# Kernel optimization log

Hardware: AMD Instinct MI355X
Metric: run time of the kernel (lower is better)

## Reference

```python
import jax, jax.numpy as jnp
import numpy as np

GROUP = 64

def dequant(W_q, scale, zero):
    # W_q: [out, in] int, scale/zero: [out, in//GROUP]
    out, din = W_q.shape
    g = din // GROUP
    Wq = W_q.reshape(out, g, GROUP).astype(scale.dtype)
    W = (Wq - zero[:, :, None]) * scale[:, :, None]
    return W.reshape(out, din)

def setup_inputs() -> dict:
    key = jax.random.key(0)
    ks = jax.random.split(key, 10)
    T, H, F = 512, 4096, 14336
    return {
        "hidden_states": jax.random.normal(ks[0], (T, H), jnp.float32),
        "W1_q": jax.random.randint(ks[1], (F, H), 0, 16, jnp.int32),
        "w1_scale": jax.random.uniform(ks[2], (F, H // GROUP), jnp.float32, 1e-3, 0.02),
        "w1_zero": jax.random.uniform(ks[3], (F, H // GROUP), jnp.float32, 6.0, 9.0),
        "W3_q": jax.random.randint(ks[4], (F, H), 0, 16, jnp.int32),
        "w3_scale": jax.random.uniform(ks[5], (F, H // GROUP), jnp.float32, 1e-3, 0.02),
        "w3_zero": jax.random.uniform(ks[6], (F, H // GROUP), jnp.float32, 6.0, 9.0),
        "W2_q": jax.random.randint(ks[7], (H, F), 0, 16, jnp.int32),
        "w2_scale": jax.random.uniform(ks[8], (H, F // GROUP), jnp.float32, 1e-3, 0.02),
        "w2_zero": jax.random.uniform(ks[9], (H, F // GROUP), jnp.float32, 6.0, 9.0),
    }

def reference(hidden_states, W1_q, w1_scale, w1_zero, W3_q, w3_scale, w3_zero, W2_q, w2_scale, w2_zero):
    W1 = dequant(W1_q, w1_scale, w1_zero)  # [F, H]
    W3 = dequant(W3_q, w3_scale, w3_zero)  # [F, H]
    W2 = dequant(W2_q, w2_scale, w2_zero)  # [H, F]
    g = jax.nn.silu(hidden_states @ W1.T) * (hidden_states @ W3.T)  # [T, F]
    return g @ W2.T  # [T, H]
```

## Files before the change

### kernel.cpp

```cpp
#include <hip/hip_runtime.h>
#include <hip/hip_bf16.h>

#define T_DIM 512
#define H_DIM 4096
#define F_DIM 14336
#define KSEG  8

typedef __attribute__((ext_vector_type(8))) short bf16x8;
typedef __attribute__((ext_vector_type(4))) float f32x4;

__device__ __forceinline__ unsigned short f2bf(float f) {
    union { __hip_bfloat16 h; unsigned short u; } cv;
    cv.h = __float2bfloat16(f);
    return cv.u;
}

__global__ __launch_bounds__(256) void zero_out(float4* __restrict__ out) {
    out[blockIdx.x * 256 + threadIdx.x] = make_float4(0.f, 0.f, 0.f, 0.f);
}

__global__ __launch_bounds__(256) void cvt_x(const float* __restrict__ X,
                                             unsigned short* __restrict__ Xb) {
    int i = (blockIdx.x * 256 + threadIdx.x) * 4;
    float4 v = *(const float4*)&X[i];
    ushort4 o;
    o.x = f2bf(v.x); o.y = f2bf(v.y); o.z = f2bf(v.z); o.w = f2bf(v.w);
    *(ushort4*)&Xb[i] = o;
}

__global__ __launch_bounds__(256, 2)
void gate_up_kernel(const unsigned short* __restrict__ Xb,
                    const int* __restrict__ W1q, const float* __restrict__ sc1,
                    const float* __restrict__ zp1,
                    const int* __restrict__ W3q, const float* __restrict__ sc3,
                    const float* __restrict__ zp3,
                    unsigned short* __restrict__ G)
{
    constexpr int LK = 72;
    __shared__ __align__(16) char smem[(128 + 64 + 64) * LK * 2];
    unsigned short* sX  = (unsigned short*)smem;
    unsigned short* sW1 = (unsigned short*)(smem + 128 * LK * 2);
    unsigned short* sW3 = (unsigned short*)(smem + 192 * LK * 2);
    float* sEx = (float*)smem;

    const int t = threadIdx.x, wave = t >> 6, lane = t & 63;
    const int r = lane & 15, q = lane >> 4;
    const int mh  = (wave & 1) * 64;
    const int mat = wave >> 1;

    const int b = blockIdx.x;
    const int xcd = b & 7, lb = b >> 3;
    const int m0 = (lb & 3) * 128;
    const int n0 = (xcd * 28 + (lb >> 2)) * 64;
    const int SG = H_DIM / 64;

    const int xrow = t >> 3, xch = (t & 7) * 8;
    const int wrow = t >> 4, wc = (t & 15) * 4;

    int4 pW1[4], pW3[4];
    #pragma unroll
    for (int i = 0; i < 4; ++i) {
        size_t off = (size_t)(n0 + wrow + 16 * i) * H_DIM + wc;
        pW1[i] = *(const int4*)&W1q[off];
        pW3[i] = *(const int4*)&W3q[off];
    }

    f32x4 acc[4][4];
    #pragma unroll
    for (int a = 0; a < 4; ++a)
        #pragma unroll
        for (int c = 0; c < 4; ++c) acc[a][c] = (f32x4){0.f, 0.f, 0.f, 0.f};

    for (int k0 = 0; k0 < H_DIM; k0 += 64) {
        const int gidx = k0 >> 6;

        #pragma unroll
        for (int i = 0; i < 4; ++i) {
            int4 xv = *(const int4*)&Xb[(size_t)(m0 + xrow + 32 * i) * H_DIM + k0 + xch];
            *(int4*)&sX[(xrow + 32 * i) * LK + xch] = xv;
        }
        #pragma unroll
        for (int i = 0; i < 4; ++i) {
            int row = wrow + 16 * i;
            int sidx = (n0 + row) * SG + gidx;
            float s = sc1[sidx], nzs = -zp1[sidx] * s;
            int4 qv = pW1[i];
            ushort4 o;
            o.x = f2bf(fmaf((float)qv.x, s, nzs)); o.y = f2bf(fmaf((float)qv.y, s, nzs));
            o.z = f2bf(fmaf((float)qv.z, s, nzs)); o.w = f2bf(fmaf((float)qv.w, s, nzs));
            *(ushort4*)&sW1[row * LK + wc] = o;
            s = sc3[sidx]; nzs = -zp3[sidx] * s;
            qv = pW3[i];
            o.x = f2bf(fmaf((float)qv.x, s, nzs)); o.y = f2bf(fmaf((float)qv.y, s, nzs));
            o.z = f2bf(fmaf((float)qv.z, s, nzs)); o.w = f2bf(fmaf((float)qv.w, s, nzs));
            *(ushort4*)&sW3[row * LK + wc] = o;
        }
        int kn = k0 + 64;
        if (kn < H_DIM) {
            #pragma unroll
            for (int i = 0; i < 4; ++i) {
                size_t off = (size_t)(n0 + wrow + 16 * i) * H_DIM + kn + wc;
                pW1[i] = *(const int4*)&W1q[off];
                pW3[i] = *(const int4*)&W3q[off];
            }
        }
        __syncthreads();

        const unsigned short* sB = mat ? sW3 : sW1;
        #pragma unroll
        for (int kh = 0; kh < 2; ++kh) {
            const int kb = kh * 32 + q * 8;
            bf16x8 av[4], bv[4];
            #pragma unroll
            for (int im = 0; im < 4; ++im)
                av[im] = *(const bf16x8*)&sX[(mh + im * 16 + r) * LK + kb];
            #pragma unroll
            for (int j = 0; j < 4; ++j)
                bv[j] = *(const bf16x8*)&sB[(j * 16 + r) * LK + kb];
            #pragma unroll
            for (int im = 0; im < 4; ++im)
                #pragma unroll
                for (int j = 0; j < 4; ++j)
                    acc[im][j] = __builtin_amdgcn_mfma_f32_16x16x32_bf16(av[im], bv[j], acc[im][j], 0, 0, 0);
        }
        __syncthreads();
    }

    if (mat == 1) {
        #pragma unroll
        for (int im = 0; im < 4; ++im)
            #pragma unroll
            for (int j = 0; j < 4; ++j)
                #pragma unroll
                for (int reg = 0; reg < 4; ++reg)
                    sEx[(mh + im * 16 + q * 4 + reg) * 65 + j * 16 + r] = acc[im][j][reg];
    }
    __syncthreads();
    if (mat == 0) {
        #pragma unroll
        for (int im = 0; im < 4; ++im)
            #pragma unroll
            for (int j = 0; j < 4; ++j)
                #pragma unroll
                for (int reg = 0; reg < 4; ++reg) {
                    int ml = mh + im * 16 + q * 4 + reg;
                    int nl = j * 16 + r;
                    float g1 = acc[im][j][reg];
                    float g3 = sEx[ml * 65 + nl];
                    float val = g1 / (1.f + __expf(-g1)) * g3;
                    G[(size_t)(m0 + ml) * F_DIM + n0 + nl] = f2bf(val);
                }
    }
}

__global__ __launch_bounds__(256, 2)
void down_kernel(const unsigned short* __restrict__ G,
                 const int* __restrict__ W2q, const float* __restrict__ sc2,
                 const float* __restrict__ zp2,
                 float* __restrict__ Out)
{
    constexpr int LK = 72;
    __shared__ __align__(16) char smem[(128 + 128) * LK * 2];
    unsigned short* sA = (unsigned short*)smem;
    unsigned short* sW = (unsigned short*)(smem + 128 * LK * 2);

    const int t = threadIdx.x, wave = t >> 6, lane = t & 63;
    const int r = lane & 15, q = lane >> 4;
    const int wm = (wave & 1) * 64, wn = (wave >> 1) * 64;

    const int b = blockIdx.x;
    const int xcd = b & 7, lb = b >> 3;
    const int m0 = (lb & 3) * 128;
    const int pair = xcd * 32 + (lb >> 2);
    const int n0 = (pair >> 3) * 128;
    const int kbeg = (pair & 7) * (F_DIM / KSEG);
    const int kend = kbeg + (F_DIM / KSEG);
    const int SG = F_DIM / 64;

    const int arow = t >> 3, ach = (t & 7) * 8;
    const int wrow = t >> 4, wc = (t & 15) * 4;

    int4 pW[8];
    #pragma unroll
    for (int i = 0; i < 8; ++i)
        pW[i] = *(const int4*)&W2q[(size_t)(n0 + wrow + 16 * i) * F_DIM + kbeg + wc];

    f32x4 acc[4][4];
    #pragma unroll
    for (int a = 0; a < 4; ++a)
        #pragma unroll
        for (int c = 0; c < 4; ++c) acc[a][c] = (f32x4){0.f, 0.f, 0.f, 0.f};

    for (int k0 = kbeg; k0 < kend; k0 += 64) {
        const int gidx = k0 >> 6;

        #pragma unroll
        for (int i = 0; i < 4; ++i) {
            int4 gv = *(const int4*)&G[(size_t)(m0 + arow + 32 * i) * F_DIM + k0 + ach];
            *(int4*)&sA[(arow + 32 * i) * LK + ach] = gv;
        }
        #pragma unroll
        for (int i = 0; i < 8; ++i) {
            int row = wrow + 16 * i;
            int sidx = (n0 + row) * SG + gidx;
            float s = sc2[sidx], nzs = -zp2[sidx] * s;
            int4 qv = pW[i];
            ushort4 o;
            o.x = f2bf(fmaf((float)qv.x, s, nzs)); o.y = f2bf(fmaf((float)qv.y, s, nzs));
            o.z = f2bf(fmaf((float)qv.z, s, nzs)); o.w = f2bf(fmaf((float)qv.w, s, nzs));
            *(ushort4*)&sW[row * LK + wc] = o;
        }
        int kn = k0 + 64;
        if (kn < kend) {
            #pragma unroll
            for (int i = 0; i < 8; ++i)
                pW[i] = *(const int4*)&W2q[(size_t)(n0 + wrow + 16 * i) * F_DIM + kn + wc];
        }
        __syncthreads();

        #pragma unroll
        for (int kh = 0; kh < 2; ++kh) {
            const int kb = kh * 32 + q * 8;
            bf16x8 av[4], bv[4];
            #pragma unroll
            for (int im = 0; im < 4; ++im)
                av[im] = *(const bf16x8*)&sA[(wm + im * 16 + r) * LK + kb];
            #pragma unroll
            for (int j = 0; j < 4; ++j)
                bv[j] = *(const bf16x8*)&sW[(wn + j * 16 + r) * LK + kb];
            #pragma unroll
            for (int im = 0; im < 4; ++im)
                #pragma unroll
                for (int j = 0; j < 4; ++j)
                    acc[im][j] = __builtin_amdgcn_mfma_f32_16x16x32_bf16(av[im], bv[j], acc[im][j], 0, 0, 0);
        }
        __syncthreads();
    }

    #pragma unroll
    for (int im = 0; im < 4; ++im)
        #pragma unroll
        for (int j = 0; j < 4; ++j)
            #pragma unroll
            for (int reg = 0; reg < 4; ++reg) {
                int m = m0 + wm + im * 16 + q * 4 + reg;
                int h = n0 + wn + j * 16 + r;
                atomicAdd(&Out[(size_t)m * H_DIM + h], acc[im][j][reg]);
            }
}

extern "C" void kernel_launch(void* const* d_in, const int* in_sizes, int n_in,
                              void* d_out, int out_size, void* d_ws, size_t ws_size,
                              hipStream_t stream) {
    const float* X   = (const float*)d_in[0];
    const int*   W1q = (const int*)d_in[1];
    const float* s1  = (const float*)d_in[2];
    const float* z1  = (const float*)d_in[3];
    const int*   W3q = (const int*)d_in[4];
    const float* s3  = (const float*)d_in[5];
    const float* z3  = (const float*)d_in[6];
    const int*   W2q = (const int*)d_in[7];
    const float* s2  = (const float*)d_in[8];
    const float* z2  = (const float*)d_in[9];
    float* Out = (float*)d_out;

    unsigned short* Xb = (unsigned short*)d_ws;
    unsigned short* G  = (unsigned short*)((char*)d_ws + (4 << 20));

    zero_out<<<2048, 256, 0, stream>>>((float4*)Out);
    cvt_x<<<2048, 256, 0, stream>>>(X, Xb);
    gate_up_kernel<<<896, 256, 0, stream>>>(Xb, W1q, s1, z1, W3q, s3, z3, G);
    down_kernel<<<1024, 256, 0, stream>>>(G, W2q, s2, z2, Out);
}
```

Measured before the change: 878.6 us.

## Double-buffer LDS tiles in gate/up and down kernels to drop one barrier

Both GEMM kernels now keep two shared-memory tile buffers. Each iteration computes MFMAs on the current buffer while loading and dequantizing the next tile into the other, so each K step needs one barrier instead of two. This should let dequant and global-load latency overlap with matrix math. It doubles LDS use per block (about 72KB for gate/up), which could limit occupancy under launch_bounds(256,2).

Measured after the change: 873.3 us. About the same (-0.6%).

```diff
diff --git a/kernel.cpp b/kernel.cpp
--- a/kernel.cpp
+++ b/kernel.cpp
@@ -13,6 +13,16 @@
     union { __hip_bfloat16 h; unsigned short u; } cv;
     cv.h = __float2bfloat16(f);
     return cv.u;
+}
+
+__device__ __forceinline__ void dq16(int4 qv, float s, float z, unsigned short* dst) {
+    float nzs = -z * s;
+    ushort4 o;
+    o.x = f2bf(fmaf((float)qv.x, s, nzs));
+    o.y = f2bf(fmaf((float)qv.y, s, nzs));
+    o.z = f2bf(fmaf((float)qv.z, s, nzs));
+    o.w = f2bf(fmaf((float)qv.w, s, nzs));
+    *(ushort4*)dst = o;
 }
 
 __global__ __launch_bounds__(256) void zero_out(float4* __restrict__ out) {
@@ -37,10 +47,8 @@
                     unsigned short* __restrict__ G)
 {
     constexpr int LK = 72;
-    __shared__ __align__(16) char smem[(128 + 64 + 64) * LK * 2];
-    unsigned short* sX  = (unsigned short*)smem;
-    unsigned short* sW1 = (unsigned short*)(smem + 128 * LK * 2);
-    unsigned short* sW3 = (unsigned short*)(smem + 192 * LK * 2);
+    constexpr int BUFB = (128 + 64 + 64) * LK * 2;
+    __shared__ __align__(16) char smem[2 * BUFB];
     float* sEx = (float*)smem;
 
     const int t = threadIdx.x, wave = t >> 6, lane = t & 63;
@@ -65,48 +73,45 @@
         pW3[i] = *(const int4*)&W3q[off];
     }
 
-    f32x4 acc[4][4];
-    #pragma unroll
-    for (int a = 0; a < 4; ++a)
-        #pragma unroll
-        for (int c = 0; c < 4; ++c) acc[a][c] = (f32x4){0.f, 0.f, 0.f, 0.f};
-
-    for (int k0 = 0; k0 < H_DIM; k0 += 64) {
-        const int gidx = k0 >> 6;
-
+    {
+        unsigned short* sX  = (unsigned short*)smem;
+        unsigned short* sW1 = (unsigned short*)(smem + 128 * LK * 2);
+        unsigned short* sW3 = (unsigned short*)(smem + 192 * LK * 2);
         #pragma unroll
         for (int i = 0; i < 4; ++i) {
-            int4 xv = *(const int4*)&Xb[(size_t)(m0 + xrow + 32 * i) * H_DIM + k0 + xch];
+            int4 xv = *(const int4*)&Xb[(size_t)(m0 + xrow + 32 * i) * H_DIM + xch];
             *(int4*)&sX[(xrow + 32 * i) * LK + xch] = xv;
         }
         #pragma unroll
         for (int i = 0; i < 4; ++i) {
             int row = wrow + 16 * i;
-            int sidx = (n0 + row) * SG + gidx;
-            float s = sc1[sidx], nzs = -zp1[sidx] * s;
-            int4 qv = pW1[i];
-            ushort4 o;
-            o.x = f2bf(fmaf((float)qv.x, s, nzs)); o.y = f2bf(fmaf((float)qv.y, s, nzs));
-            o.z = f2bf(fmaf((float)qv.z, s, nzs)); o.w = f2bf(fmaf((float)qv.w, s, nzs));
-            *(ushort4*)&sW1[row * LK + wc] = o;
-            s = sc3[sidx]; nzs = -zp3[sidx] * s;
-            qv = pW3[i];
-            o.x = f2bf(fmaf((float)qv.x, s, nzs)); o.y = f2bf(fmaf((float)qv.y, s, nzs));
-            o.z = f2bf(fmaf((float)qv.z, s, nzs)); o.w = f2bf(fmaf((float)qv.w, s, nzs));
-            *(ushort4*)&sW3[row * LK + wc] = o;
-        }
-        int kn = k0 + 64;
-        if (kn < H_DIM) {
-            #pragma unroll
-            for (int i = 0; i < 4; ++i) {
-                size_t off = (size_t)(n0 + wrow + 16 * i) * H_DIM + kn + wc;
-                pW1[i] = *(const int4*)&W1q[off];
-                pW3[i] = *(const int4*)&W3q[off];
-            }
-        }
-        __syncthreads();
-
-        const unsigned short* sB = mat ? sW3 : sW1;
+            int sidx = (n0 + row) * SG;
+            dq16(pW1[i], sc1[sidx], zp1[sidx], &sW1[row * LK + wc]);
+            dq16(pW3[i], sc3[sidx], zp3[sidx], &sW3[row * LK + wc]);
+        }
+        #pragma unroll
+        for (int i = 0; i < 4; ++i) {
+            size_t off = (size_t)(n0 + wrow + 16 * i) * H_DIM + 64 + wc;
+            pW1[i] = *(const int4*)&W1q[off];
+            pW3[i] = *(const int4*)&W3q[off];
+        }
+    }
+    __syncthreads();
+
+    f32x4 acc[4][4];
+    #pragma unroll
+    for (int a = 0; a < 4; ++a)
+        #pragma unroll
+        for (int c = 0; c < 4; ++c) acc[a][c] = (f32x4){0.f, 0.f, 0.f, 0.f};
+
+    constexpr int NIT = H_DIM / 64;
+    #pragma unroll 2
+    for (int it = 0; it < NIT; ++it) {
+        const char* cb = smem + (it & 1) * BUFB;
+        const unsigned short* sX = (const unsigned short*)cb;
+        const unsigned short* sB =
+            (const unsigned short*)(cb + (mat ? 192 : 128) * LK * 2);
+
         #pragma unroll
         for (int kh = 0; kh < 2; ++kh) {
             const int kb = kh * 32 + q * 8;
@@ -123,7 +128,37 @@
                 for (int j = 0; j < 4; ++j)
                     acc[im][j] = __builtin_amdgcn_mfma_f32_16x16x32_bf16(av[im], bv[j], acc[im][j], 0, 0, 0);
         }
-        __syncthreads();
+
+        if (it < NIT - 1) {
+            char* nb = smem + ((it + 1) & 1) * BUFB;
+            unsigned short* nX  = (unsigned short*)nb;
+            unsigned short* nW1 = (unsigned short*)(nb + 128 * LK * 2);
+            unsigned short* nW3 = (unsigned short*)(nb + 192 * LK * 2);
+            const int kn = (it + 1) * 64;
+            #pragma unroll
+            for (int i = 0; i < 4; ++i) {
+                int4 xv = *(const int4*)&Xb[(size_t)(m0 + xrow + 32 * i) * H_DIM + kn + xch];
+                *(int4*)&nX[(xrow + 32 * i) * LK + xch] = xv;
+            }
+            const int gidx = it + 1;
+            #pragma unroll
+            for (int i = 0; i < 4; ++i) {
+                int row = wrow + 16 * i;
+                int sidx = (n0 + row) * SG + gidx;
+                dq16(pW1[i], sc1[sidx], zp1[sidx], &nW1[row * LK + wc]);
+                dq16(pW3[i], sc3[sidx], zp3[sidx], &nW3[row * LK + wc]);
+            }
+            if (it < NIT - 2) {
+                const int kf = (it + 2) * 64;
+                #pragma unroll
+                for (int i = 0; i < 4; ++i) {
+                    size_t off = (size_t)(n0 + wrow + 16 * i) * H_DIM + kf + wc;
+                    pW1[i] = *(const int4*)&W1q[off];
+                    pW3[i] = *(const int4*)&W3q[off];
+                }
+            }
+            __syncthreads();
+        }
     }
 
     if (mat == 1) {
@@ -160,9 +195,8 @@
                  float* __restrict__ Out)
 {
     constexpr int LK = 72;
-    __shared__ __align__(16) char smem[(128 + 128) * LK * 2];
-    unsigned short* sA = (unsigned short*)smem;
-    unsigned short* sW = (unsigned short*)(smem + 128 * LK * 2);
+    constexpr int BUFB = (128 + 128) * LK * 2;
+    __shared__ __align__(16) char smem[2 * BUFB];
 
     const int t = threadIdx.x, wave = t >> 6, lane = t & 63;
     const int r = lane & 15, q = lane >> 4;
@@ -174,7 +208,6 @@
     const int pair = xcd * 32 + (lb >> 2);
     const int n0 = (pair >> 3) * 128;
     const int kbeg = (pair & 7) * (F_DIM / KSEG);
-    const int kend = kbeg + (F_DIM / KSEG);
     const int SG = F_DIM / 64;
 
     const int arow = t >> 3, ach = (t & 7) * 8;
@@ -185,38 +218,39 @@
     for (int i = 0; i < 8; ++i)
         pW[i] = *(const int4*)&W2q[(size_t)(n0 + wrow + 16 * i) * F_DIM + kbeg + wc];
 
-    f32x4 acc[4][4];
-    #pragma unroll
-    for (int a = 0; a < 4; ++a)
-        #pragma unroll
-        for (int c = 0; c < 4; ++c) acc[a][c] = (f32x4){0.f, 0.f, 0.f, 0.f};
-
-    for (int k0 = kbeg; k0 < kend; k0 += 64) {
-        const int gidx = k0 >> 6;
-
+    {
+        unsigned short* sA = (unsigned short*)smem;
+        unsigned short* sW = (unsigned short*)(smem + 128 * LK * 2);
         #pragma unroll
         for (int i = 0; i < 4; ++i) {
-            int4 gv = *(const int4*)&G[(size_t)(m0 + arow + 32 * i) * F_DIM + k0 + ach];
+            int4 gv = *(const int4*)&G[(size_t)(m0 + arow + 32 * i) * F_DIM + kbeg + ach];
             *(int4*)&sA[(arow + 32 * i) * LK + ach] = gv;
         }
+        const int gidx = kbeg >> 6;
         #pragma unroll
         for (int i = 0; i < 8; ++i) {
             int row = wrow + 16 * i;
             int sidx = (n0 + row) * SG + gidx;
-            float s = sc2[sidx], nzs = -zp2[sidx] * s;
-            int4 qv = pW[i];
-            ushort4 o;
-            o.x = f2bf(fmaf((float)qv.x, s, nzs)); o.y = f2bf(fmaf((float)qv.y, s, nzs));
-            o.z = f2bf(fmaf((float)qv.z, s, nzs)); o.w = f2bf(fmaf((float)qv.w, s, nzs));
-            *(ushort4*)&sW[row * LK + wc] = o;
-        }
-        int kn = k0 + 64;
-        if (kn < kend) {
-            #pragma unroll
-            for (int i = 0; i < 8; ++i)
-                pW[i] = *(const int4*)&W2q[(size_t)(n0 + wrow + 16 * i) * F_DIM + kn + wc];
-        }
-        __syncthreads();
+            dq16(pW[i], sc2[sidx], zp2[sidx], &sW[row * LK + wc]);
+        }
+        #pragma unroll
+        for (int i = 0; i < 8; ++i)
+            pW[i] = *(const int4*)&W2q[(size_t)(n0 + wrow + 16 * i) * F_DIM + kbeg + 64 + wc];
+    }
+    __syncthreads();
+
+    f32x4 acc[4][4];
+    #pragma unroll
+    for (int a = 0; a < 4; ++a)
+        #pragma unroll
+        for (int c = 0; c < 4; ++c) acc[a][c] = (f32x4){0.f, 0.f, 0.f, 0.f};
+
+    constexpr int NIT = (F_DIM / KSEG) / 64;
+    #pragma unroll 2
+    for (int it = 0; it < NIT; ++it) {
+        const char* cb = smem + (it & 1) * BUFB;
+        const unsigned short* sA = (const unsigned short*)cb;
+        const unsigned short* sW = (const unsigned short*)(cb + 128 * LK * 2);
 
         #pragma unroll
         for (int kh = 0; kh < 2; ++kh) {
@@ -234,7 +268,32 @@
                 for (int j = 0; j < 4; ++j)
                     acc[im][j] = __builtin_amdgcn_mfma_f32_16x16x32_bf16(av[im], bv[j], acc[im][j], 0, 0, 0);
         }
-        __syncthreads();
+
+        if (it < NIT - 1) {
+            char* nb = smem + ((it + 1) & 1) * BUFB;
+            unsigned short* nA = (unsigned short*)nb;
+            unsigned short* nW = (unsigned short*)(nb + 128 * LK * 2);
+            const int kn = kbeg + (it + 1) * 64;
+            #pragma unroll
+            for (int i = 0; i < 4; ++i) {
+                int4 gv = *(const int4*)&G[(size_t)(m0 + arow + 32 * i) * F_DIM + kn + ach];
+                *(int4*)&nA[(arow + 32 * i) * LK + ach] = gv;
+            }
+            const int gidx = kn >> 6;
+            #pragma unroll
+            for (int i = 0; i < 8; ++i) {
+                int row = wrow + 16 * i;
+                int sidx = (n0 + row) * SG + gidx;
+                dq16(pW[i], sc2[sidx], zp2[sidx], &nW[row * LK + wc]);
+            }
+            if (it < NIT - 2) {
+                const int kf = kbeg + (it + 2) * 64;
+                #pragma unroll
+                for (int i = 0; i < 8; ++i)
+                    pW[i] = *(const int4*)&W2q[(size_t)(n0 + wrow + 16 * i) * F_DIM + kf + wc];
+            }
+            __syncthreads();
+        }
     }
 
     #pragma unroll
```
